# Performance work log

Hardware: AMD Instinct MI355X
Metric: run time of the kernel (lower is better)

Reference implementation:

```python
import jax, jax.numpy as jnp
import numpy as np

B, K, T = 64, 256, 64      # batch, num_tokens (feature dim of e / Dense units), word tokens
DF, N = 768, 1024          # image feature channels, spatial regions


def setup_inputs() -> dict:
    key = jax.random.key(0)
    k1, k2, k3 = jax.random.split(key, 3)
    e = jax.random.normal(k1, (B, K, T), dtype=jnp.float32)
    f = jax.random.normal(k2, (B, DF, N), dtype=jnp.float32)
    # Dense(units=K) kernel/bias (Glorot-ish scale)
    W = jax.random.normal(k3, (DF, K), dtype=jnp.float32) / np.sqrt(DF)
    b = jnp.zeros((K,), dtype=jnp.float32)
    gamma = jnp.float32(5.0)  # DAMSM smoothing factor gamma1
    return {"e": e, "f": f, "gamma": gamma, "W": W, "b": b}


def reference(e, f, gamma, W, b):
    # v = transpose(Dense(transpose(f))): project image features Df -> K. [B,K,N]
    v = jnp.einsum('bdn,dk->bkn', f, W) + b[None, :, None]
    # attention scores between word tokens and regions: [B,T,N]
    s = jnp.einsum('bkt,bkn->btn', e, v)
    # gamma-scaled softmax over regions (axis=2)
    alpha = jax.nn.softmax(gamma * s, axis=2)
    # region-context vectors per token: [B,K,T]
    c = jnp.einsum('bkn,btn->bkt', v, alpha)
    # per-token feature norms (reduce over feature axis 1): [B,T]
    lc = jnp.sqrt(jnp.sum(c * c, axis=1))
    le = jnp.sqrt(jnp.sum(e * e, axis=1))
    # token-token cosine similarity: contract feature axis, normalize by outer(lc, le)
    cos = jnp.einsum('bki,bkj->bij', c, e) / (lc[:, :, None] * le[:, None, :])
    return cos
```

## Files before the change

### kernel.cpp

```cpp
#include <hip/hip_runtime.h>

#define B_  64
#define K_  256
#define T_  64
#define DF_ 768
#define N_  1024

typedef __attribute__((ext_vector_type(8))) short bf16x8;
typedef __attribute__((ext_vector_type(4))) float f32x4;

__device__ __forceinline__ unsigned short bf_rne(float x) {
    unsigned u = __float_as_uint(x);
    unsigned r = u + 0x7fffu + ((u >> 16) & 1u);
    return (unsigned short)(r >> 16);
}

__global__ __launch_bounds__(256) void prep_we(const float* __restrict__ W,
                                               const float* __restrict__ e,
                                               unsigned short* __restrict__ W_hi,
                                               unsigned short* __restrict__ W_lo,
                                               unsigned short* __restrict__ WT_hi,
                                               unsigned short* __restrict__ eT_hi,
                                               unsigned short* __restrict__ eT_lo) {
    int blk = blockIdx.x;
    if (blk < DF_) {
        int d = blk, k = threadIdx.x;
        float w = W[d * K_ + k];
        unsigned u = __float_as_uint(w);
        unsigned short hs = (unsigned short)(u >> 16);
        float hi = __uint_as_float(u & 0xffff0000u);
        W_hi[d * K_ + k]   = hs;
        W_lo[d * K_ + k]   = bf_rne(w - hi);
        WT_hi[k * DF_ + d] = hs;
    } else {
        int q = blk - DF_;
        int b = q >> 2, kq = q & 3;
        int t = threadIdx.x & 63, ko = threadIdx.x >> 6;
        const float* eb = e + (size_t)b * K_ * T_;
        unsigned short* eh = eT_hi + (size_t)b * T_ * K_;
        unsigned short* el = eT_lo + (size_t)b * T_ * K_;
#pragma unroll
        for (int i = 0; i < 16; i++) {
            int k = kq * 64 + ko * 16 + i;
            float x = eb[k * T_ + t];
            unsigned u = __float_as_uint(x);
            unsigned short hs = (unsigned short)(u >> 16);
            float hi = __uint_as_float(u & 0xffff0000u);
            eh[t * K_ + k] = hs;
            el[t * K_ + k] = bf_rne(x - hi);
        }
    }
}

__global__ __launch_bounds__(256, 2) void gemm_g(const unsigned short* __restrict__ eT_hi,
                                                 const unsigned short* __restrict__ eT_lo,
                                                 const unsigned short* __restrict__ W_hi,
                                                 const unsigned short* __restrict__ W_lo,
                                                 unsigned short* __restrict__ gT_hi,
                                                 unsigned short* __restrict__ gT_lo) {
    __shared__ unsigned short LeH[64 * 40], LeL[64 * 40];
    __shared__ unsigned short LwH[64 * 40], LwL[64 * 40];
    const int dblk = blockIdx.x * 64;
    const int b = blockIdx.y;
    const int tid = threadIdx.x;
    const int lane = tid & 63, w = tid >> 6, q = lane >> 4, l16 = lane & 15;

    const unsigned short* eh = eT_hi + (size_t)b * T_ * K_;
    const unsigned short* el = eT_lo + (size_t)b * T_ * K_;

    f32x4 acc[4];
#pragma unroll
    for (int i = 0; i < 4; i++) acc[i] = (f32x4)(0.f);

    const int tr = tid >> 2, c8 = (tid & 3) * 8;
    for (int k0 = 0; k0 < K_; k0 += 32) {
        *(uint4*)&LeH[tr * 40 + c8] = *(const uint4*)&eh[tr * K_ + k0 + c8];
        *(uint4*)&LeL[tr * 40 + c8] = *(const uint4*)&el[tr * K_ + k0 + c8];
        *(uint4*)&LwH[tr * 40 + c8] = *(const uint4*)&W_hi[(size_t)(dblk + tr) * K_ + k0 + c8];
        *(uint4*)&LwL[tr * 40 + c8] = *(const uint4*)&W_lo[(size_t)(dblk + tr) * K_ + k0 + c8];
        __syncthreads();
        bf16x8 aH[4], aL[4], bH, bL;
#pragma unroll
        for (int mt = 0; mt < 4; mt++) {
            aH[mt] = *(const bf16x8*)&LeH[(mt * 16 + l16) * 40 + q * 8];
            aL[mt] = *(const bf16x8*)&LeL[(mt * 16 + l16) * 40 + q * 8];
        }
        int dl = w * 16 + l16;
        bH = *(const bf16x8*)&LwH[dl * 40 + q * 8];
        bL = *(const bf16x8*)&LwL[dl * 40 + q * 8];
#pragma unroll
        for (int mt = 0; mt < 4; mt++) {
            acc[mt] = __builtin_amdgcn_mfma_f32_16x16x32_bf16(aH[mt], bH, acc[mt], 0, 0, 0);
            acc[mt] = __builtin_amdgcn_mfma_f32_16x16x32_bf16(aH[mt], bL, acc[mt], 0, 0, 0);
            acc[mt] = __builtin_amdgcn_mfma_f32_16x16x32_bf16(aL[mt], bH, acc[mt], 0, 0, 0);
        }
        __syncthreads();
    }

    unsigned short* gh = gT_hi + (size_t)b * T_ * DF_;
    unsigned short* gl = gT_lo + (size_t)b * T_ * DF_;
#pragma unroll
    for (int mt = 0; mt < 4; mt++)
#pragma unroll
        for (int r = 0; r < 4; r++) {
            float x = acc[mt][r];
            int t = mt * 16 + q * 4 + r;
            int d = dblk + w * 16 + l16;
            unsigned u = __float_as_uint(x);
            unsigned short hs = (unsigned short)(u >> 16);
            float hi = __uint_as_float(u & 0xffff0000u);
            gh[t * DF_ + d] = hs;
            gl[t * DF_ + d] = bf_rne(x - hi);
        }
}

__global__ __launch_bounds__(256, 2) void gemm_s(const unsigned short* __restrict__ gT_hi,
                                                 const unsigned short* __restrict__ gT_lo,
                                                 const float* __restrict__ f,
                                                 float* __restrict__ s) {
    __shared__ unsigned short LgH[2][64 * 40], LgL[2][64 * 40];
    __shared__ unsigned LfH[2][128 * 20], LfL[2][128 * 20];

    const int flat = blockIdx.x;
    const int b    = (flat & 7) * 8 + ((flat >> 3) & 7);
    const int nblk = (flat >> 6) * 128;
    const int tid = threadIdx.x;
    const int lane = tid & 63, w = tid >> 6, q = lane >> 4, l16 = lane & 15;

    const unsigned short* gh = gT_hi + (size_t)b * T_ * DF_;
    const unsigned short* gl = gT_lo + (size_t)b * T_ * DF_;

    f32x4 acc[4][2];
#pragma unroll
    for (int i = 0; i < 4; i++)
#pragma unroll
        for (int j = 0; j < 2; j++) acc[i][j] = (f32x4)(0.f);

    const int dp  = tid >> 4;
    const int nb  = (tid & 15) * 8;
    const int rot = tid & 7;
    const int tr = tid >> 2, c8 = (tid & 3) * 8;

    const float* fbase = f + ((size_t)b * DF_ + dp * 2) * N_ + nblk + nb;
    const unsigned short* ghp = gh + (size_t)tr * DF_ + c8;
    const unsigned short* glp = gl + (size_t)tr * DF_ + c8;

    float4 px0, px1, py0, py1;
    uint4 pgH, pgL;

    auto sload = [&](int d0) {
        const float* fp = fbase + (size_t)d0 * N_;
        px0 = *(const float4*)&fp[0];
        px1 = *(const float4*)&fp[4];
        py0 = *(const float4*)&fp[N_ + 0];
        py1 = *(const float4*)&fp[N_ + 4];
        pgH = *(const uint4*)&ghp[d0];
        pgL = *(const uint4*)&glp[d0];
    };
    auto sstore = [&](int buf) {
        *(uint4*)&LgH[buf][tr * 40 + c8] = pgH;
        *(uint4*)&LgL[buf][tr * 40 + c8] = pgL;
        const float xs[8] = {px0.x, px0.y, px0.z, px0.w, px1.x, px1.y, px1.z, px1.w};
        const float ys[8] = {py0.x, py0.y, py0.z, py0.w, py1.x, py1.y, py1.z, py1.w};
#pragma unroll
        for (int jj = 0; jj < 8; jj++) {
            int j = (jj + rot) & 7;
            unsigned bx = __float_as_uint(xs[j]);
            unsigned by = __float_as_uint(ys[j]);
            unsigned hp = (bx >> 16) | (by & 0xffff0000u);
            float lx = xs[j] - __uint_as_float(bx & 0xffff0000u);
            float ly = ys[j] - __uint_as_float(by & 0xffff0000u);
            unsigned lp = (__float_as_uint(lx) >> 16) | (__float_as_uint(ly) & 0xffff0000u);
            LfH[buf][(nb + j) * 20 + dp] = hp;
            LfL[buf][(nb + j) * 20 + dp] = lp;
        }
    };
    auto scomp = [&](int buf) {
        bf16x8 aH[4], aL[4], bH[2], bL[2];
#pragma unroll
        for (int mt = 0; mt < 4; mt++) {
            aH[mt] = *(const bf16x8*)&LgH[buf][(mt * 16 + l16) * 40 + q * 8];
            aL[mt] = *(const bf16x8*)&LgL[buf][(mt * 16 + l16) * 40 + q * 8];
        }
#pragma unroll
        for (int nt = 0; nt < 2; nt++) {
            int nl = w * 32 + nt * 16 + l16;
            bH[nt] = *(const bf16x8*)&((const unsigned short*)LfH[buf])[nl * 40 + q * 8];
            bL[nt] = *(const bf16x8*)&((const unsigned short*)LfL[buf])[nl * 40 + q * 8];
        }
#pragma unroll
        for (int mt = 0; mt < 4; mt++)
#pragma unroll
            for (int nt = 0; nt < 2; nt++) {
                acc[mt][nt] = __builtin_amdgcn_mfma_f32_16x16x32_bf16(aH[mt], bH[nt], acc[mt][nt], 0, 0, 0);
                acc[mt][nt] = __builtin_amdgcn_mfma_f32_16x16x32_bf16(aH[mt], bL[nt], acc[mt][nt], 0, 0, 0);
                acc[mt][nt] = __builtin_amdgcn_mfma_f32_16x16x32_bf16(aL[mt], bH[nt], acc[mt][nt], 0, 0, 0);
            }
    };

    sload(0);
    sstore(0);
    __syncthreads();
    int cur = 0;
    for (int d0 = 0; d0 < DF_ - 32; d0 += 32) {
        sload(d0 + 32);
        scomp(cur);
        sstore(cur ^ 1);
        __syncthreads();
        cur ^= 1;
    }
    scomp(cur);

    float* sb = s + (size_t)b * T_ * N_;
#pragma unroll
    for (int mt = 0; mt < 4; mt++)
#pragma unroll
        for (int nt = 0; nt < 2; nt++)
#pragma unroll
            for (int r = 0; r < 4; r++) {
                int t = mt * 16 + q * 4 + r;
                int n = nblk + w * 32 + nt * 16 + l16;
                sb[(size_t)t * N_ + n] = acc[mt][nt][r];
            }
}

__global__ __launch_bounds__(256) void softmax_k(const float* __restrict__ s,
                                                 unsigned short* __restrict__ alpha,
                                                 const float* __restrict__ gptr) {
    const float g = gptr[0];
    const int row_id = blockIdx.x * 4 + (threadIdx.x >> 6);
    const int lane = threadIdx.x & 63;
    const float* row = s + (size_t)row_id * N_;
    unsigned short* arow = alpha + (size_t)row_id * N_;

    float4 x[4];
#pragma unroll
    for (int i = 0; i < 4; i++) {
        x[i] = *(const float4*)(row + i * 256 + lane * 4);
        x[i].x *= g; x[i].y *= g; x[i].z *= g; x[i].w *= g;
    }
    float m = x[0].x;
#pragma unroll
    for (int i = 0; i < 4; i++)
        m = fmaxf(m, fmaxf(fmaxf(x[i].x, x[i].y), fmaxf(x[i].z, x[i].w)));
#pragma unroll
    for (int off = 32; off > 0; off >>= 1) m = fmaxf(m, __shfl_xor(m, off, 64));

    float ev[16];
    float sum = 0.f;
#pragma unroll
    for (int i = 0; i < 4; i++) {
        ev[i * 4 + 0] = __expf(x[i].x - m);
        ev[i * 4 + 1] = __expf(x[i].y - m);
        ev[i * 4 + 2] = __expf(x[i].z - m);
        ev[i * 4 + 3] = __expf(x[i].w - m);
        sum += ev[i * 4 + 0] + ev[i * 4 + 1] + ev[i * 4 + 2] + ev[i * 4 + 3];
    }
#pragma unroll
    for (int off = 32; off > 0; off >>= 1) sum += __shfl_xor(sum, off, 64);
    float inv = 1.f / sum;
#pragma unroll
    for (int i = 0; i < 4; i++) {
        unsigned p0 = (unsigned)bf_rne(ev[i * 4 + 0] * inv) | ((unsigned)bf_rne(ev[i * 4 + 1] * inv) << 16);
        unsigned p1 = (unsigned)bf_rne(ev[i * 4 + 2] * inv) | ((unsigned)bf_rne(ev[i * 4 + 3] * inv) << 16);
        uint2 o; o.x = p0; o.y = p1;
        *(uint2*)&arow[i * 256 + lane * 4] = o;
    }
}

__global__ __launch_bounds__(256, 2) void gemm_h(const float* __restrict__ f,
                                                 const unsigned short* __restrict__ alpha,
                                                 unsigned short* __restrict__ hT) {
    __shared__ unsigned short Lf[2][64 * 72];
    __shared__ unsigned short La[2][64 * 72];
    const int dblk = blockIdx.x * 64;
    const int b = blockIdx.y;
    const int tid = threadIdx.x;
    const int lane = tid & 63, w = tid >> 6, q = lane >> 4, l16 = lane & 15;

    const float* fb = f + (size_t)b * DF_ * N_;
    const unsigned short* ab = alpha + (size_t)b * T_ * N_;

    f32x4 acc[4];
#pragma unroll
    for (int i = 0; i < 4; i++) acc[i] = (f32x4)(0.f);

    const int fr_ = tid >> 2, fc = tid & 3;
    const float* frbase = fb + (size_t)(dblk + fr_) * N_ + fc * 16;
    const unsigned short* abase = ab + (size_t)fr_ * N_ + fc * 16;

    float4 pf0, pf1, pf2, pf3;
    uint4 pa0, pa1;

    auto hload = [&](int n0) {
        const float* fp = frbase + n0;
        pf0 = *(const float4*)&fp[0];
        pf1 = *(const float4*)&fp[4];
        pf2 = *(const float4*)&fp[8];
        pf3 = *(const float4*)&fp[12];
        pa0 = *(const uint4*)&abase[n0];
        pa1 = *(const uint4*)&abase[n0 + 8];
    };
    auto hstore = [&](int buf) {
        const float4 fx[4] = {pf0, pf1, pf2, pf3};
#pragma unroll
        for (int i = 0; i < 4; i++) {
            float4 x = fx[i];
            unsigned p0 = (unsigned)bf_rne(x.x) | ((unsigned)bf_rne(x.y) << 16);
            unsigned p1 = (unsigned)bf_rne(x.z) | ((unsigned)bf_rne(x.w) << 16);
            uint2 o; o.x = p0; o.y = p1;
            *(uint2*)&Lf[buf][fr_ * 72 + fc * 16 + i * 4] = o;
        }
        *(uint4*)&La[buf][fr_ * 72 + fc * 16]     = pa0;
        *(uint4*)&La[buf][fr_ * 72 + fc * 16 + 8] = pa1;
    };
    auto hcomp = [&](int buf) {
        bf16x8 af[2], bb[4][2];
#pragma unroll
        for (int kk = 0; kk < 2; kk++)
            af[kk] = *(const bf16x8*)&Lf[buf][(w * 16 + l16) * 72 + kk * 32 + q * 8];
#pragma unroll
        for (int nt = 0; nt < 4; nt++)
#pragma unroll
            for (int kk = 0; kk < 2; kk++)
                bb[nt][kk] = *(const bf16x8*)&La[buf][(nt * 16 + l16) * 72 + kk * 32 + q * 8];
#pragma unroll
        for (int nt = 0; nt < 4; nt++)
#pragma unroll
            for (int kk = 0; kk < 2; kk++)
                acc[nt] = __builtin_amdgcn_mfma_f32_16x16x32_bf16(af[kk], bb[nt][kk], acc[nt], 0, 0, 0);
    };

    hload(0);
    hstore(0);
    __syncthreads();
    int cur = 0;
    for (int n0 = 0; n0 < N_ - 64; n0 += 64) {
        hload(n0 + 64);
        hcomp(cur);
        hstore(cur ^ 1);
        __syncthreads();
        cur ^= 1;
    }
    hcomp(cur);

    unsigned short* hb = hT + (size_t)b * T_ * DF_;
#pragma unroll
    for (int nt = 0; nt < 4; nt++)
#pragma unroll
        for (int r = 0; r < 4; r++) {
            int d = dblk + w * 16 + q * 4 + r;
            int t = nt * 16 + l16;
            hb[(size_t)t * DF_ + d] = bf_rne(acc[nt][r]);
        }
}

__global__ __launch_bounds__(256, 2) void gemm_c(const unsigned short* __restrict__ WT_hi,
                                                 const unsigned short* __restrict__ hT,
                                                 const float* __restrict__ bias,
                                                 float* __restrict__ c) {
    __shared__ unsigned short LW[64 * 72];
    __shared__ unsigned short Lh[64 * 72];
    const int kblk = blockIdx.x * 64;
    const int b = blockIdx.y;
    const int tid = threadIdx.x;
    const int lane = tid & 63, w = tid >> 6, q = lane >> 4, l16 = lane & 15;

    const unsigned short* hb = hT + (size_t)b * T_ * DF_;

    f32x4 acc[4];
#pragma unroll
    for (int i = 0; i < 4; i++) acc[i] = (f32x4)(0.f);

    for (int d0 = 0; d0 < DF_; d0 += 64) {
#pragma unroll
        for (int l = 0; l < 2; l++) {
            int idx = tid * 2 + l;
            int r = idx >> 3, c8 = (idx & 7) * 8;
            *(uint4*)&LW[r * 72 + c8] = *(const uint4*)&WT_hi[(size_t)(kblk + r) * DF_ + d0 + c8];
            *(uint4*)&Lh[r * 72 + c8] = *(const uint4*)&hb[(size_t)r * DF_ + d0 + c8];
        }
        __syncthreads();
        bf16x8 aw[2], bh[4][2];
#pragma unroll
        for (int kk = 0; kk < 2; kk++)
            aw[kk] = *(const bf16x8*)&LW[(w * 16 + l16) * 72 + kk * 32 + q * 8];
#pragma unroll
        for (int nt = 0; nt < 4; nt++)
#pragma unroll
            for (int kk = 0; kk < 2; kk++)
                bh[nt][kk] = *(const bf16x8*)&Lh[(nt * 16 + l16) * 72 + kk * 32 + q * 8];
#pragma unroll
        for (int nt = 0; nt < 4; nt++)
#pragma unroll
            for (int kk = 0; kk < 2; kk++)
                acc[nt] = __builtin_amdgcn_mfma_f32_16x16x32_bf16(aw[kk], bh[nt][kk], acc[nt], 0, 0, 0);
        __syncthreads();
    }

    float* cb = c + (size_t)b * K_ * T_;
#pragma unroll
    for (int nt = 0; nt < 4; nt++)
#pragma unroll
        for (int r = 0; r < 4; r++) {
            int k = kblk + w * 16 + q * 4 + r;
            int t = nt * 16 + l16;
            cb[(size_t)k * T_ + t] = acc[nt][r] + bias[k];
        }
}

__global__ __launch_bounds__(256) void cos_k(const float* __restrict__ c,
                                             const float* __restrict__ e,
                                             float* __restrict__ out) {
    const int iq = threadIdx.x >> 6;
    const int i = blockIdx.x * 4 + iq;
    const int b = blockIdx.y;
    const int j = threadIdx.x & 63;
    const float* cb = c + (size_t)b * K_ * T_;
    const float* eb = e + (size_t)b * K_ * T_;

    float dot = 0.f, se = 0.f, sc = 0.f;
#pragma unroll 8
    for (int k = 0; k < K_; k++) {
        float cv = cb[(size_t)k * T_ + i];
        float ev = eb[(size_t)k * T_ + j];
        dot += cv * ev;
        se  += ev * ev;
        sc  += cv * cv;
    }
    out[((size_t)b * T_ + i) * T_ + j] = dot * rsqrtf(sc * se);
}

extern "C" void kernel_launch(void* const* d_in, const int* in_sizes, int n_in,
                              void* d_out, int out_size, void* d_ws, size_t ws_size,
                              hipStream_t stream) {
    const float* e     = (const float*)d_in[0];
    const float* f     = (const float*)d_in[1];
    const float* gamma = (const float*)d_in[2];
    const float* W     = (const float*)d_in[3];
    const float* bias  = (const float*)d_in[4];
    float* out = (float*)d_out;

    char* p = (char*)d_ws;
    unsigned short* W_hi  = (unsigned short*)p; p += (size_t)DF_ * K_ * 2;
    unsigned short* W_lo  = (unsigned short*)p; p += (size_t)DF_ * K_ * 2;
    unsigned short* WT_hi = (unsigned short*)p; p += (size_t)DF_ * K_ * 2;
    unsigned short* eT_hi = (unsigned short*)p; p += (size_t)B_ * T_ * K_ * 2;
    unsigned short* eT_lo = (unsigned short*)p; p += (size_t)B_ * T_ * K_ * 2;
    unsigned short* gT_hi = (unsigned short*)p; p += (size_t)B_ * T_ * DF_ * 2;
    unsigned short* gT_lo = (unsigned short*)p; p += (size_t)B_ * T_ * DF_ * 2;
    float*          s     = (float*)p;          p += (size_t)B_ * T_ * N_ * 4;
    unsigned short* alpha = (unsigned short*)p; p += (size_t)B_ * T_ * N_ * 2;
    unsigned short* hT    = (unsigned short*)p; p += (size_t)B_ * T_ * DF_ * 2;
    float*          c     = (float*)p;          p += (size_t)B_ * K_ * T_ * 4;

    prep_we <<<dim3(DF_ + 256),      256, 0, stream>>>(W, e, W_hi, W_lo, WT_hi, eT_hi, eT_lo);
    gemm_g  <<<dim3(DF_ / 64, B_),   256, 0, stream>>>(eT_hi, eT_lo, W_hi, W_lo, gT_hi, gT_lo);
    gemm_s  <<<dim3(512),            256, 0, stream>>>(gT_hi, gT_lo, f, s);
    softmax_k<<<dim3(B_ * T_ / 4),   256, 0, stream>>>(s, alpha, gamma);
    gemm_h  <<<dim3(DF_ / 64, B_),   256, 0, stream>>>(f, alpha, hT);
    gemm_c  <<<dim3(K_ / 64, B_),    256, 0, stream>>>(WT_hi, hT, bias, c);
    cos_k   <<<dim3(T_ / 4, B_),     256, 0, stream>>>(c, e, out);
}
```

Measured before the change: 374.9 us.

## Double-buffer gemm_g/gemm_c, load g fragments from global in gemm_s

gemm_g and gemm_c switch to register-prefetched, double-buffered LDS tiles, so each next tile's global loads overlap the current tile's MFMAs and one barrier per iteration is dropped. gemm_s stops staging the g operand through LDS and loads MFMA fragments straight from global memory into registers, prefetched one step ahead. Launch bounds for gemm_g and gemm_h go up to three blocks per CU to allow more waves in flight. The costs are more registers and LDS per block, which may limit occupancy, and uncoalesced strided global fragment loads in gemm_s.

```diff
diff --git a/kernel.cpp b/kernel.cpp
--- a/kernel.cpp
+++ b/kernel.cpp
@@ -52,14 +52,14 @@
     }
 }
 
-__global__ __launch_bounds__(256, 2) void gemm_g(const unsigned short* __restrict__ eT_hi,
+__global__ __launch_bounds__(256, 3) void gemm_g(const unsigned short* __restrict__ eT_hi,
                                                  const unsigned short* __restrict__ eT_lo,
                                                  const unsigned short* __restrict__ W_hi,
                                                  const unsigned short* __restrict__ W_lo,
                                                  unsigned short* __restrict__ gT_hi,
                                                  unsigned short* __restrict__ gT_lo) {
-    __shared__ unsigned short LeH[64 * 40], LeL[64 * 40];
-    __shared__ unsigned short LwH[64 * 40], LwL[64 * 40];
+    __shared__ unsigned short LeH[2][64 * 40], LeL[2][64 * 40];
+    __shared__ unsigned short LwH[2][64 * 40], LwL[2][64 * 40];
     const int dblk = blockIdx.x * 64;
     const int b = blockIdx.y;
     const int tid = threadIdx.x;
@@ -73,29 +73,54 @@
     for (int i = 0; i < 4; i++) acc[i] = (f32x4)(0.f);
 
     const int tr = tid >> 2, c8 = (tid & 3) * 8;
-    for (int k0 = 0; k0 < K_; k0 += 32) {
-        *(uint4*)&LeH[tr * 40 + c8] = *(const uint4*)&eh[tr * K_ + k0 + c8];
-        *(uint4*)&LeL[tr * 40 + c8] = *(const uint4*)&el[tr * K_ + k0 + c8];
-        *(uint4*)&LwH[tr * 40 + c8] = *(const uint4*)&W_hi[(size_t)(dblk + tr) * K_ + k0 + c8];
-        *(uint4*)&LwL[tr * 40 + c8] = *(const uint4*)&W_lo[(size_t)(dblk + tr) * K_ + k0 + c8];
-        __syncthreads();
+    const unsigned short* ehp = eh + (size_t)tr * K_ + c8;
+    const unsigned short* elp = el + (size_t)tr * K_ + c8;
+    const unsigned short* whp = W_hi + (size_t)(dblk + tr) * K_ + c8;
+    const unsigned short* wlp = W_lo + (size_t)(dblk + tr) * K_ + c8;
+
+    uint4 peH, peL, pwH, pwL;
+    auto gload = [&](int k0) {
+        peH = *(const uint4*)&ehp[k0];
+        peL = *(const uint4*)&elp[k0];
+        pwH = *(const uint4*)&whp[k0];
+        pwL = *(const uint4*)&wlp[k0];
+    };
+    auto gstore = [&](int buf) {
+        *(uint4*)&LeH[buf][tr * 40 + c8] = peH;
+        *(uint4*)&LeL[buf][tr * 40 + c8] = peL;
+        *(uint4*)&LwH[buf][tr * 40 + c8] = pwH;
+        *(uint4*)&LwL[buf][tr * 40 + c8] = pwL;
+    };
+    auto gcomp = [&](int buf) {
         bf16x8 aH[4], aL[4], bH, bL;
 #pragma unroll
         for (int mt = 0; mt < 4; mt++) {
-            aH[mt] = *(const bf16x8*)&LeH[(mt * 16 + l16) * 40 + q * 8];
-            aL[mt] = *(const bf16x8*)&LeL[(mt * 16 + l16) * 40 + q * 8];
+            aH[mt] = *(const bf16x8*)&LeH[buf][(mt * 16 + l16) * 40 + q * 8];
+            aL[mt] = *(const bf16x8*)&LeL[buf][(mt * 16 + l16) * 40 + q * 8];
         }
         int dl = w * 16 + l16;
-        bH = *(const bf16x8*)&LwH[dl * 40 + q * 8];
-        bL = *(const bf16x8*)&LwL[dl * 40 + q * 8];
+        bH = *(const bf16x8*)&LwH[buf][dl * 40 + q * 8];
+        bL = *(const bf16x8*)&LwL[buf][dl * 40 + q * 8];
 #pragma unroll
         for (int mt = 0; mt < 4; mt++) {
             acc[mt] = __builtin_amdgcn_mfma_f32_16x16x32_bf16(aH[mt], bH, acc[mt], 0, 0, 0);
             acc[mt] = __builtin_amdgcn_mfma_f32_16x16x32_bf16(aH[mt], bL, acc[mt], 0, 0, 0);
             acc[mt] = __builtin_amdgcn_mfma_f32_16x16x32_bf16(aL[mt], bH, acc[mt], 0, 0, 0);
         }
+    };
+
+    gload(0);
+    gstore(0);
+    __syncthreads();
+    int cur = 0;
+    for (int k0 = 0; k0 < K_ - 32; k0 += 32) {
+        gload(k0 + 32);
+        gcomp(cur);
+        gstore(cur ^ 1);
         __syncthreads();
-    }
+        cur ^= 1;
+    }
+    gcomp(cur);
 
     unsigned short* gh = gT_hi + (size_t)b * T_ * DF_;
     unsigned short* gl = gT_lo + (size_t)b * T_ * DF_;
@@ -118,7 +143,6 @@
                                                  const unsigned short* __restrict__ gT_lo,
                                                  const float* __restrict__ f,
                                                  float* __restrict__ s) {
-    __shared__ unsigned short LgH[2][64 * 40], LgL[2][64 * 40];
     __shared__ unsigned LfH[2][128 * 20], LfL[2][128 * 20];
 
     const int flat = blockIdx.x;
@@ -139,27 +163,20 @@
     const int dp  = tid >> 4;
     const int nb  = (tid & 15) * 8;
     const int rot = tid & 7;
-    const int tr = tid >> 2, c8 = (tid & 3) * 8;
 
     const float* fbase = f + ((size_t)b * DF_ + dp * 2) * N_ + nblk + nb;
-    const unsigned short* ghp = gh + (size_t)tr * DF_ + c8;
-    const unsigned short* glp = gl + (size_t)tr * DF_ + c8;
+    const unsigned short* gfh = gh + (size_t)l16 * DF_ + q * 8;
+    const unsigned short* gfl = gl + (size_t)l16 * DF_ + q * 8;
 
     float4 px0, px1, py0, py1;
-    uint4 pgH, pgL;
-
     auto sload = [&](int d0) {
         const float* fp = fbase + (size_t)d0 * N_;
         px0 = *(const float4*)&fp[0];
         px1 = *(const float4*)&fp[4];
         py0 = *(const float4*)&fp[N_ + 0];
         py1 = *(const float4*)&fp[N_ + 4];
-        pgH = *(const uint4*)&ghp[d0];
-        pgL = *(const uint4*)&glp[d0];
     };
     auto sstore = [&](int buf) {
-        *(uint4*)&LgH[buf][tr * 40 + c8] = pgH;
-        *(uint4*)&LgL[buf][tr * 40 + c8] = pgL;
         const float xs[8] = {px0.x, px0.y, px0.z, px0.w, px1.x, px1.y, px1.z, px1.w};
         const float ys[8] = {py0.x, py0.y, py0.z, py0.w, py1.x, py1.y, py1.z, py1.w};
 #pragma unroll
@@ -175,13 +192,15 @@
             LfL[buf][(nb + j) * 20 + dp] = lp;
         }
     };
-    auto scomp = [&](int buf) {
-        bf16x8 aH[4], aL[4], bH[2], bL[2];
+    auto gfrag = [&](bf16x8 (&H)[4], bf16x8 (&L)[4], int d0) {
 #pragma unroll
         for (int mt = 0; mt < 4; mt++) {
-            aH[mt] = *(const bf16x8*)&LgH[buf][(mt * 16 + l16) * 40 + q * 8];
-            aL[mt] = *(const bf16x8*)&LgL[buf][(mt * 16 + l16) * 40 + q * 8];
-        }
+            H[mt] = *(const bf16x8*)&gfh[(size_t)(mt * 16) * DF_ + d0];
+            L[mt] = *(const bf16x8*)&gfl[(size_t)(mt * 16) * DF_ + d0];
+        }
+    };
+    auto scomp = [&](int buf, const bf16x8 (&aH)[4], const bf16x8 (&aL)[4]) {
+        bf16x8 bH[2], bL[2];
 #pragma unroll
         for (int nt = 0; nt < 2; nt++) {
             int nl = w * 32 + nt * 16 + l16;
@@ -198,18 +217,23 @@
             }
     };
 
+    bf16x8 aH[4], aL[4], nH[4], nL[4];
     sload(0);
+    gfrag(aH, aL, 0);
     sstore(0);
     __syncthreads();
     int cur = 0;
     for (int d0 = 0; d0 < DF_ - 32; d0 += 32) {
         sload(d0 + 32);
-        scomp(cur);
+        gfrag(nH, nL, d0 + 32);
+        scomp(cur, aH, aL);
         sstore(cur ^ 1);
         __syncthreads();
+#pragma unroll
+        for (int i = 0; i < 4; i++) { aH[i] = nH[i]; aL[i] = nL[i]; }
         cur ^= 1;
     }
-    scomp(cur);
+    scomp(cur, aH, aL);
 
     float* sb = s + (size_t)b * T_ * N_;
 #pragma unroll
@@ -268,7 +292,7 @@
     }
 }
 
-__global__ __launch_bounds__(256, 2) void gemm_h(const float* __restrict__ f,
+__global__ __launch_bounds__(256, 3) void gemm_h(const float* __restrict__ f,
                                                  const unsigned short* __restrict__ alpha,
                                                  unsigned short* __restrict__ hT) {
     __shared__ unsigned short Lf[2][64 * 72];
@@ -359,8 +383,8 @@
                                                  const unsigned short* __restrict__ hT,
                                                  const float* __restrict__ bias,
                                                  float* __restrict__ c) {
-    __shared__ unsigned short LW[64 * 72];
-    __shared__ unsigned short Lh[64 * 72];
+    __shared__ unsigned short LW[2][64 * 72];
+    __shared__ unsigned short Lh[2][64 * 72];
     const int kblk = blockIdx.x * 64;
     const int b = blockIdx.y;
     const int tid = threadIdx.x;
@@ -372,31 +396,52 @@
 #pragma unroll
     for (int i = 0; i < 4; i++) acc[i] = (f32x4)(0.f);
 
-    for (int d0 = 0; d0 < DF_; d0 += 64) {
-#pragma unroll
-        for (int l = 0; l < 2; l++) {
-            int idx = tid * 2 + l;
-            int r = idx >> 3, c8 = (idx & 7) * 8;
-            *(uint4*)&LW[r * 72 + c8] = *(const uint4*)&WT_hi[(size_t)(kblk + r) * DF_ + d0 + c8];
-            *(uint4*)&Lh[r * 72 + c8] = *(const uint4*)&hb[(size_t)r * DF_ + d0 + c8];
-        }
-        __syncthreads();
+    const int r_ = tid >> 2, cc = (tid & 3) * 16;
+    const unsigned short* wbase = WT_hi + (size_t)(kblk + r_) * DF_ + cc;
+    const unsigned short* hbase = hb + (size_t)r_ * DF_ + cc;
+
+    uint4 pw0, pw1, ph0, ph1;
+    auto cload = [&](int d0) {
+        pw0 = *(const uint4*)&wbase[d0];
+        pw1 = *(const uint4*)&wbase[d0 + 8];
+        ph0 = *(const uint4*)&hbase[d0];
+        ph1 = *(const uint4*)&hbase[d0 + 8];
+    };
+    auto cstore = [&](int buf) {
+        *(uint4*)&LW[buf][r_ * 72 + cc]     = pw0;
+        *(uint4*)&LW[buf][r_ * 72 + cc + 8] = pw1;
+        *(uint4*)&Lh[buf][r_ * 72 + cc]     = ph0;
+        *(uint4*)&Lh[buf][r_ * 72 + cc + 8] = ph1;
+    };
+    auto ccomp = [&](int buf) {
         bf16x8 aw[2], bh[4][2];
 #pragma unroll
         for (int kk = 0; kk < 2; kk++)
-            aw[kk] = *(const bf16x8*)&LW[(w * 16 + l16) * 72 + kk * 32 + q * 8];
+            aw[kk] = *(const bf16x8*)&LW[buf][(w * 16 + l16) * 72 + kk * 32 + q * 8];
 #pragma unroll
         for (int nt = 0; nt < 4; nt++)
 #pragma unroll
             for (int kk = 0; kk < 2; kk++)
-                bh[nt][kk] = *(const bf16x8*)&Lh[(nt * 16 + l16) * 72 + kk * 32 + q * 8];
+                bh[nt][kk] = *(const bf16x8*)&Lh[buf][(nt * 16 + l16) * 72 + kk * 32 + q * 8];
 #pragma unroll
         for (int nt = 0; nt < 4; nt++)
 #pragma unroll
             for (int kk = 0; kk < 2; kk++)
                 acc[nt] = __builtin_amdgcn_mfma_f32_16x16x32_bf16(aw[kk], bh[nt][kk], acc[nt], 0, 0, 0);
+    };
+
+    cload(0);
+    cstore(0);
+    __syncthreads();
+    int cur = 0;
+    for (int d0 = 0; d0 < DF_ - 64; d0 += 64) {
+        cload(d0 + 64);
+        ccomp(cur);
+        cstore(cur ^ 1);
         __syncthreads();
-    }
+        cur ^= 1;
+    }
+    ccomp(cur);
 
     float* cb = c + (size_t)b * K_ * T_;
 #pragma unroll
```

Result: slower. 389.8 us (+3.9%).
